# Performance work log

Hardware: AMD Instinct MI355X
Metric: run time of the kernel (lower is better)

## Reference

```python
import jax, jax.numpy as jnp
import numpy as np

N = 50000      # nodes
E = 800000     # edges (before self-loops)
IN = 64        # in_channels
H = 4          # heads
C = 32         # out_channels per head
HC = H * C     # 128
NEG_SLOPE = 0.2


def setup_inputs() -> dict:
    key = jax.random.key(0)
    ks = jax.random.split(key, 16)
    def p(k, shape):
        return (jax.random.normal(k, shape, jnp.float32) * 0.1)
    x = jax.random.normal(ks[0], (N, IN), jnp.float32)
    edge_index = jax.random.randint(ks[1], (2, E), 0, N, dtype=jnp.int32)
    return {
        "x": x,
        "Wl1": p(ks[2], (IN, HC)),  "bl1": p(ks[3], (HC,)),
        "Wr1": p(ks[4], (IN, HC)),  "br1": p(ks[5], (HC,)),
        "att1": p(ks[6], (H, C)),   "bias1": p(ks[7], (HC,)),
        "Wl2": p(ks[8], (HC, HC)),  "bl2": p(ks[9], (HC,)),
        "Wr2": p(ks[10], (HC, HC)), "br2": p(ks[11], (HC,)),
        "att2": p(ks[12], (H, C)),  "bias2": p(ks[13], (HC,)),
        "edge_index": edge_index,
    }


def gatv2_layer(x, src, dst, Wl, bl, Wr, br, att, bias):
    """GATv2Conv (concat=True, eval mode). src/dst include self-loops."""
    n = x.shape[0]
    h, c = att.shape
    xl = (x @ Wl + bl).reshape(n, h, c)   # source-side transform
    xr = (x @ Wr + br).reshape(n, h, c)   # target-side transform
    # per-edge GATv2 score: att . LeakyReLU(x_j + x_i)
    e = jax.nn.leaky_relu(xl[src] + xr[dst], NEG_SLOPE)   # [E', H, C]
    score = jnp.einsum('ehc,hc->eh', e, att)              # [E', H]
    # segment softmax over destination node
    m = jax.ops.segment_max(score, dst, num_segments=n)   # [N, H]
    ex = jnp.exp(score - m[dst])
    denom = jax.ops.segment_sum(ex, dst, num_segments=n)  # [N, H]
    alpha = ex / denom[dst]                               # [E', H]
    # weighted scatter-aggregate of source messages
    out = jax.ops.segment_sum(alpha[:, :, None] * xl[src], dst, num_segments=n)
    return out.reshape(n, h * c) + bias


def reference(x, Wl1, bl1, Wr1, br1, att1, bias1,
              Wl2, bl2, Wr2, br2, att2, bias2, edge_index):
    n = x.shape[0]
    loops = jnp.arange(n, dtype=edge_index.dtype)
    src = jnp.concatenate([edge_index[0], loops])  # PyG add_self_loops=True
    dst = jnp.concatenate([edge_index[1], loops])
    h = jax.nn.relu(gatv2_layer(x, src, dst, Wl1, bl1, Wr1, br1, att1, bias1))
    out = jax.nn.relu(gatv2_layer(h, src, dst, Wl2, bl2, Wr2, br2, att2, bias2))
    return out
```

## Files before the change

kernel.cpp:

```cpp
#include <hip/hip_runtime.h>

#define LEAKY 0.2f
#define NBSHIFT 8
#define TILE 4096

typedef __attribute__((ext_vector_type(8))) short  bfrag;
typedef __attribute__((ext_vector_type(4))) float  f32x4;

__device__ __forceinline__ unsigned bf16rne(float v) {
    unsigned u = __float_as_uint(v);
    return (u + 0x7FFF + ((u >> 16) & 1)) >> 16;
}
__device__ __forceinline__ float bf16tof(unsigned b) { return __uint_as_float(b << 16); }

#define DPPADD(p, ctrl)                                                       \
    p += __int_as_float(__builtin_amdgcn_mov_dpp(__float_as_int(p), ctrl,     \
                                                 0xF, 0xF, true))
__device__ __forceinline__ float rowsum8(float p) {
    DPPADD(p, 0xB1);
    DPPADD(p, 0x4E);
    DPPADD(p, 0x141);
    return p;
}


__global__ __launch_bounds__(256) void bucket_hist(const int* __restrict__ dst,
                                                   int* __restrict__ bcnt, int E, int nb) {
    __shared__ int h[256];
    h[threadIdx.x] = 0;
    __syncthreads();
    for (int e = blockIdx.x * 256 + threadIdx.x; e < E; e += gridDim.x * 256)
        atomicAdd(&h[dst[e] >> NBSHIFT], 1);
    __syncthreads();
    int v = h[threadIdx.x];
    if (threadIdx.x < nb && v) atomicAdd(&bcnt[threadIdx.x], v);
}

__global__ __launch_bounds__(256) void bucket_scan(const int* __restrict__ bcnt,
                                                   int* __restrict__ bbase,
                                                   int* __restrict__ gwoff,
                                                   int* __restrict__ rowptr,
                                                   int E, int nb, int n) {
    __shared__ int s[256];
    const int t = threadIdx.x;
    int v = (t < nb) ? bcnt[t] : 0;
    s[t] = v;
    __syncthreads();
    for (int off = 1; off < 256; off <<= 1) {
        int a = (t >= off) ? s[t - off] : 0;
        __syncthreads();
        s[t] += a;
        __syncthreads();
    }
    int excl = s[t] - v;
    if (t < nb) { bbase[t] = excl; gwoff[t] = excl; }
    if (t == 0) { bbase[nb] = E; rowptr[n] = E; }
}

__global__ __launch_bounds__(256) void multisplit(const int* __restrict__ src,
                                                  const int* __restrict__ dst,
                                                  int* __restrict__ gwoff,
                                                  int* __restrict__ pairs, int E, int nb) {
    __shared__ int hist[256], lofs[256], gb[256];
    __shared__ int st[TILE];
    const int t = threadIdx.x;
    const int tile0 = blockIdx.x * TILE;
    const int tend = min(tile0 + TILE, E);
    hist[t] = 0;
    __syncthreads();
    for (int e = tile0 + t; e < tend; e += 256)
        atomicAdd(&hist[dst[e] >> NBSHIFT], 1);
    __syncthreads();
    int v = hist[t];
    lofs[t] = v;
    __syncthreads();
    for (int off = 1; off < 256; off <<= 1) {
        int a = (t >= off) ? lofs[t - off] : 0;
        __syncthreads();
        lofs[t] += a;
        __syncthreads();
    }
    int excl = lofs[t] - v;
    __syncthreads();
    lofs[t] = excl;
    if (t < nb && v > 0) gb[t] = atomicAdd(&gwoff[t], v);
    hist[t] = 0;
    __syncthreads();
    for (int e = tile0 + t; e < tend; e += 256) {
        int d = dst[e];
        int b = d >> NBSHIFT;
        int r = atomicAdd(&hist[b], 1);
        st[lofs[b] + r] = (src[e] & 0xFFFF) | ((d & 255) << 16) | (b << 24);
    }
    __syncthreads();
    const int total = tend - tile0;
    for (int i = t; i < total; i += 256) {
        int p = st[i];
        int b = ((unsigned)p) >> 24;
        pairs[gb[b] + (i - lofs[b])] = p;
    }
}

__global__ __launch_bounds__(256) void bucket_sort(const int* __restrict__ pairs,
                                                   const int* __restrict__ bbase,
                                                   int* __restrict__ rowptr,
                                                   int* __restrict__ ssrc, int n) {
    __shared__ int hist[256], ofs[256];
    const int b = blockIdx.x, t = threadIdx.x;
    const int base = b << NBSHIFT;
    const int pbeg = bbase[b], pend = bbase[b + 1];
    hist[t] = 0;
    __syncthreads();
    for (int i = pbeg + t; i < pend; i += 256)
        atomicAdd(&hist[(pairs[i] >> 16) & 255], 1);
    __syncthreads();
    int v = hist[t];
    ofs[t] = v;
    __syncthreads();
    for (int off = 1; off < 256; off <<= 1) {
        int a = (t >= off) ? ofs[t - off] : 0;
        __syncthreads();
        ofs[t] += a;
        __syncthreads();
    }
    int excl = ofs[t] - v;
    __syncthreads();
    ofs[t] = excl;
    const int node = base + t;
    if (node < n) rowptr[node] = pbeg + excl;
    __syncthreads();
    for (int i = pbeg + t; i < pend; i += 256) {
        int p = pairs[i];
        int pos = atomicAdd(&ofs[(p >> 16) & 255], 1);
        ssrc[pbeg + pos] = p & 0xFFFF;
    }
}


__global__ void split_x(const float* __restrict__ x, ushort* __restrict__ xhi,
                        ushort* __restrict__ xlo, int total4) {
    int i = blockIdx.x * blockDim.x + threadIdx.x;
    if (i >= total4) return;
    float4 v = reinterpret_cast<const float4*>(x)[i];
    ushort4 h, l;
    float* vp = &v.x;
    ushort* hp = &h.x;
    ushort* lp = &l.x;
#pragma unroll
    for (int j = 0; j < 4; ++j) {
        unsigned hb = bf16rne(vp[j]);
        hp[j] = (ushort)hb;
        lp[j] = (ushort)bf16rne(vp[j] - bf16tof(hb));
    }
    reinterpret_cast<ushort4*>(xhi)[i] = h;
    reinterpret_cast<ushort4*>(xlo)[i] = l;
}


__global__ void pack_W(const float* __restrict__ Wl, const float* __restrict__ Wr,
                       ushort* __restrict__ Bhi, ushort* __restrict__ Blo, int K) {
    int tid = blockIdx.x * blockDim.x + threadIdx.x;
    if (tid >= K * 256) return;
    int k = tid >> 8;
    int c = tid & 255;
    float w = (c < 128) ? Wl[k * 128 + c] : Wr[k * 128 + (c - 128)];
    int s = k >> 5, kin = k & 31, kgrp = kin >> 3, j = kin & 7;
    int f = c >> 4, cin = c & 15;
    int lane = kgrp * 16 + cin;
    size_t pos = ((size_t)(s * 16 + f) * 64 + lane) * 8 + j;
    unsigned hb = bf16rne(w);
    Bhi[pos] = (ushort)hb;
    Blo[pos] = (ushort)bf16rne(w - bf16tof(hb));
}


template<int K>
__global__ __launch_bounds__(256) void gemm_mfma(
    const ushort* __restrict__ Ahi, const ushort* __restrict__ Alo,
    const ushort* __restrict__ Bhi, const ushort* __restrict__ Blo,
    const float* __restrict__ bl, const float* __restrict__ br,
    ushort* __restrict__ xlb, ushort* __restrict__ xrb, int n)
{
    __shared__ ushort BshH[2 * 8 * 64 * 8];
    __shared__ ushort BshL[2 * 8 * 64 * 8];
    const int t = threadIdx.x;
    const int w = t >> 6;
    const int lane = t & 63;
    const int half = blockIdx.y;
    const int r0 = blockIdx.x * 64 + w * 16;
    const int rl = lane & 15;
    const int kg = lane >> 4;
    int arow = r0 + rl; if (arow >= n) arow = 0;

    const float4* __restrict__ gH = reinterpret_cast<const float4*>(Bhi);
    const float4* __restrict__ gL = reinterpret_cast<const float4*>(Blo);
    float4* __restrict__ sH = reinterpret_cast<float4*>(BshH);
    float4* __restrict__ sL = reinterpret_cast<float4*>(BshL);

    f32x4 acc[8];
#pragma unroll
    for (int f = 0; f < 8; ++f) acc[f] = (f32x4){0.f, 0.f, 0.f, 0.f};

#pragma unroll
    for (int sg = 0; sg < K / 64; ++sg) {
        if (sg) __syncthreads();
#pragma unroll
        for (int i = t; i < 1024; i += 256) {
            int ss = i >> 9, fl = (i >> 6) & 7, ln = i & 63;
            int gidx = ((2 * sg + ss) * 16 + half * 8 + fl) * 64 + ln;
            sH[i] = gH[gidx];
            sL[i] = gL[gidx];
        }
        __syncthreads();

#pragma unroll
        for (int ss = 0; ss < 2; ++ss) {
            const int s = 2 * sg + ss;
            const size_t ao = (size_t)arow * K + s * 32 + kg * 8;
            bfrag ahi = *reinterpret_cast<const bfrag*>(&Ahi[ao]);
            bfrag alo = *reinterpret_cast<const bfrag*>(&Alo[ao]);
#pragma unroll
            for (int fl = 0; fl < 8; ++fl) {
                const int lofs = ((ss * 8 + fl) * 64 + lane) * 8;
                bfrag bhi = *reinterpret_cast<const bfrag*>(&BshH[lofs]);
                bfrag blo = *reinterpret_cast<const bfrag*>(&BshL[lofs]);
                acc[fl] = __builtin_amdgcn_mfma_f32_16x16x32_bf16(alo, bhi, acc[fl], 0, 0, 0);
                acc[fl] = __builtin_amdgcn_mfma_f32_16x16x32_bf16(ahi, blo, acc[fl], 0, 0, 0);
                acc[fl] = __builtin_amdgcn_mfma_f32_16x16x32_bf16(ahi, bhi, acc[fl], 0, 0, 0);
            }
        }
    }

    const int cin = lane & 15;
    const float* __restrict__ bias_ = half ? br : bl;
    ushort* __restrict__ outp = half ? xrb : xlb;
#pragma unroll
    for (int fl = 0; fl < 8; ++fl) {
        const int cc = fl * 16 + cin;
        const float bv = bias_[cc];
#pragma unroll
        for (int j = 0; j < 4; ++j) {
            const int rr = r0 + kg * 4 + j;
            if (rr < n)
                outp[(size_t)rr * 128 + cc] = (ushort)bf16rne(acc[fl][j] + bv);
        }
    }
}


template<int OUTMODE>
__global__ __launch_bounds__(256) void gat_agg(
    const ushort* __restrict__ xlb, const ushort* __restrict__ xrb,
    const float* __restrict__ att, const float* __restrict__ bias,
    const int* __restrict__ rowptr, const int* __restrict__ ssrc,
    float* __restrict__ out, ushort* __restrict__ ohi, ushort* __restrict__ olo,
    int n)
{
    const int node = blockIdx.x * 4 + (threadIdx.x >> 6);
    if (node >= n) return;
    const int lane = threadIdx.x & 63;
    const int m = lane & 31;
    const bool hiHalf = lane >= 32;

    const uint2* __restrict__ xlu = reinterpret_cast<const uint2*>(xlb);
    const float4 a4 = reinterpret_cast<const float4*>(att)[m];
    float4 xrv;
    {
        const uint2 u = reinterpret_cast<const uint2*>(xrb)[(size_t)node * 32 + m];
        xrv.x = __uint_as_float(u.x << 16);
        xrv.y = __uint_as_float(u.x & 0xFFFF0000u);
        xrv.z = __uint_as_float(u.y << 16);
        xrv.w = __uint_as_float(u.y & 0xFFFF0000u);
    }

    float den = 0.f;
    float4 acc = make_float4(0.f, 0.f, 0.f, 0.f);

#define GATHER(sA, sB) xlu[(size_t)(hiHalf ? (sB) : (sA)) * 32 + m]
#define PAIR(u, MSK)                                                  \
    {                                                                 \
        const float x0 = __uint_as_float((u).x << 16);                \
        const float x1 = __uint_as_float((u).x & 0xFFFF0000u);        \
        const float x2 = __uint_as_float((u).y << 16);                \
        const float x3 = __uint_as_float((u).y & 0xFFFF0000u);        \
        float e0 = x0 + xrv.x, e1 = x1 + xrv.y;                       \
        float e2 = x2 + xrv.z, e3 = x3 + xrv.w;                       \
        e0 = fmaxf(e0, LEAKY * e0);                                   \
        e1 = fmaxf(e1, LEAKY * e1);                                   \
        e2 = fmaxf(e2, LEAKY * e2);                                   \
        e3 = fmaxf(e3, LEAKY * e3);                                   \
        float p = e0 * a4.x + e1 * a4.y + e2 * a4.z + e3 * a4.w;      \
        p = rowsum8(p);                                               \
        float ex = __expf(p) MSK;                                     \
        den += ex;                                                    \
        acc.x += ex * x0; acc.y += ex * x1;                           \
        acc.z += ex * x2; acc.w += ex * x3;                           \
    }

    int i = rowptr[node];
    const int end = rowptr[node + 1];

    {
        const bool vB = i < end;
        const int sB = vB ? ssrc[i] : node;
        uint2 u = GATHER(node, sB);
        const float msk = (hiHalf && !vB) ? 0.f : 1.f;
        PAIR(u, * msk);
        if (vB) ++i;
    }

    for (; i + 8 <= end; i += 8) {
        int s0 = ssrc[i],     s1 = ssrc[i + 1], s2 = ssrc[i + 2], s3 = ssrc[i + 3];
        int s4 = ssrc[i + 4], s5 = ssrc[i + 5], s6 = ssrc[i + 6], s7 = ssrc[i + 7];
        uint2 u0 = GATHER(s0, s1);
        uint2 u1 = GATHER(s2, s3);
        uint2 u2 = GATHER(s4, s5);
        uint2 u3 = GATHER(s6, s7);
        PAIR(u0, );
        PAIR(u1, );
        PAIR(u2, );
        PAIR(u3, );
    }
    for (; i + 2 <= end; i += 2) {
        int s0 = ssrc[i], s1 = ssrc[i + 1];
        uint2 u = GATHER(s0, s1);
        PAIR(u, );
    }
    if (i < end) {
        int s0 = ssrc[i];
        uint2 u = GATHER(s0, s0);
        const float msk = hiHalf ? 0.f : 1.f;
        PAIR(u, * msk);
    }
#undef PAIR
#undef GATHER

    den   += __shfl_xor(den,   32);
    acc.x += __shfl_xor(acc.x, 32);
    acc.y += __shfl_xor(acc.y, 32);
    acc.z += __shfl_xor(acc.z, 32);
    acc.w += __shfl_xor(acc.w, 32);

    if (!hiHalf) {
        const float4 b4 = reinterpret_cast<const float4*>(bias)[m];
        const float r = 1.f / den;
        const float o0 = fmaxf(acc.x * r + b4.x, 0.f);
        const float o1 = fmaxf(acc.y * r + b4.y, 0.f);
        const float o2 = fmaxf(acc.z * r + b4.z, 0.f);
        const float o3 = fmaxf(acc.w * r + b4.w, 0.f);
        if (OUTMODE == 0) {
            reinterpret_cast<float4*>(out)[(size_t)node * 32 + m] =
                make_float4(o0, o1, o2, o3);
        } else {
            unsigned h0 = bf16rne(o0), h1 = bf16rne(o1);
            unsigned h2 = bf16rne(o2), h3 = bf16rne(o3);
            ushort4 hv = make_ushort4((ushort)h0, (ushort)h1, (ushort)h2, (ushort)h3);
            ushort4 lv = make_ushort4((ushort)bf16rne(o0 - bf16tof(h0)),
                                      (ushort)bf16rne(o1 - bf16tof(h1)),
                                      (ushort)bf16rne(o2 - bf16tof(h2)),
                                      (ushort)bf16rne(o3 - bf16tof(h3)));
            reinterpret_cast<ushort4*>(ohi)[(size_t)node * 32 + m] = hv;
            reinterpret_cast<ushort4*>(olo)[(size_t)node * 32 + m] = lv;
        }
    }
}


extern "C" void kernel_launch(void* const* d_in, const int* in_sizes, int n_in,
                              void* d_out, int out_size, void* d_ws, size_t ws_size,
                              hipStream_t stream)
{
    const float* x     = (const float*)d_in[0];
    const float* Wl1   = (const float*)d_in[1];
    const float* bl1   = (const float*)d_in[2];
    const float* Wr1   = (const float*)d_in[3];
    const float* br1   = (const float*)d_in[4];
    const float* att1  = (const float*)d_in[5];
    const float* bias1 = (const float*)d_in[6];
    const float* Wl2   = (const float*)d_in[7];
    const float* bl2   = (const float*)d_in[8];
    const float* Wr2   = (const float*)d_in[9];
    const float* br2   = (const float*)d_in[10];
    const float* att2  = (const float*)d_in[11];
    const float* bias2 = (const float*)d_in[12];
    const int*   eidx  = (const int*)d_in[13];

    const int n = in_sizes[0] / 64;
    const int E = in_sizes[13] / 2;
    const int* src = eidx;
    const int* dst = eidx + E;
    const int nb = (n + 255) >> 8;

    char* ws = (char*)d_ws;
    size_t off = 0;
    auto alloc = [&](size_t bytes) -> void* {
        void* p = ws + off;
        off = (off + bytes + 255) & ~(size_t)255;
        return p;
    };
    int* rowptr   = (int*)alloc((size_t)(n + 1) * 4);
    int* ssrc     = (int*)alloc((size_t)E * 4);
    int* bcnt     = (int*)alloc((size_t)nb * 4);
    int* bbase    = (int*)alloc((size_t)(nb + 1) * 4);
    int* gwoff    = (int*)alloc((size_t)nb * 4);
    ushort* B1hi  = (ushort*)alloc((size_t)64  * 256 * 2);
    ushort* B1lo  = (ushort*)alloc((size_t)64  * 256 * 2);
    ushort* B2hi  = (ushort*)alloc((size_t)128 * 256 * 2);
    ushort* B2lo  = (ushort*)alloc((size_t)128 * 256 * 2);
    ushort* xreg  = (ushort*)alloc((size_t)n * 128 * 2 * 2);
    ushort* xhi1  = xreg;
    ushort* xlo1  = xreg + (size_t)n * 64;
    ushort* hhi   = xreg;
    ushort* hlo   = xreg + (size_t)n * 128;
    ushort* xlb   = (ushort*)alloc((size_t)n * 128 * 2);
    ushort* xrb   = (ushort*)alloc((size_t)n * 128 * 2);
    int* pairs    = (int*)xlb;
    float* outp   = (float*)d_out;

    hipMemsetAsync(bcnt, 0, (size_t)nb * 4, stream);
    bucket_hist<<<128, 256, 0, stream>>>(dst, bcnt, E, nb);
    bucket_scan<<<1, 256, 0, stream>>>(bcnt, bbase, gwoff, rowptr, E, nb, n);
    multisplit<<<(E + TILE - 1) / TILE, 256, 0, stream>>>(src, dst, gwoff, pairs, E, nb);
    bucket_sort<<<nb, 256, 0, stream>>>(pairs, bbase, rowptr, ssrc, n);

    const int total4 = n * 64 / 4;
    split_x<<<(total4 + 255) / 256, 256, 0, stream>>>(x, xhi1, xlo1, total4);
    pack_W<<<(64  * 256 + 255) / 256, 256, 0, stream>>>(Wl1, Wr1, B1hi, B1lo, 64);
    pack_W<<<(128 * 256 + 255) / 256, 256, 0, stream>>>(Wl2, Wr2, B2hi, B2lo, 128);

    const dim3 ggrid((n + 63) / 64, 2);

    gemm_mfma<64><<<ggrid, 256, 0, stream>>>(xhi1, xlo1, B1hi, B1lo, bl1, br1,
                                             xlb, xrb, n);
    gat_agg<1><<<(n + 3) / 4, 256, 0, stream>>>(xlb, xrb, att1, bias1, rowptr, ssrc,
                                                nullptr, hhi, hlo, n);

    gemm_mfma<128><<<ggrid, 256, 0, stream>>>(hhi, hlo, B2hi, B2lo, bl2, br2,
                                              xlb, xrb, n);
    gat_agg<0><<<(n + 3) / 4, 256, 0, stream>>>(xlb, xrb, att2, bias2, rowptr, ssrc,
                                                outp, nullptr, nullptr, n);
}
```

Baseline: 193.0 us.

## Store layer-1 output as single bf16 and merge GEMM column halves per block

Layer-1 aggregation now writes the hidden activations as a single bf16 array instead of a hi/lo bf16 pair. The second GEMM therefore drops the A-low MFMA term, saving a third of its MFMAs and half of its A reads. The GEMM also covers both Wl and Wr column halves in one 512-thread block, so each A row is fetched once per block and the y-dimension of the grid goes away. The aggregation loop gains a 16-edge unrolled stage to put more gathers in flight, at the cost of lower precision in the layer-2 input.

```diff
diff --git a/kernel.cpp b/kernel.cpp
--- a/kernel.cpp
+++ b/kernel.cpp
@@ -174,20 +174,21 @@
 }
 
 
-template<int K>
-__global__ __launch_bounds__(256) void gemm_mfma(
+template<int K, bool SPLITA>
+__global__ __launch_bounds__(512) void gemm_mfma(
     const ushort* __restrict__ Ahi, const ushort* __restrict__ Alo,
     const ushort* __restrict__ Bhi, const ushort* __restrict__ Blo,
     const float* __restrict__ bl, const float* __restrict__ br,
     ushort* __restrict__ xlb, ushort* __restrict__ xrb, int n)
 {
-    __shared__ ushort BshH[2 * 8 * 64 * 8];
-    __shared__ ushort BshL[2 * 8 * 64 * 8];
+    __shared__ ushort BshH[2 * 16 * 64 * 8];
+    __shared__ ushort BshL[2 * 16 * 64 * 8];
     const int t = threadIdx.x;
     const int w = t >> 6;
     const int lane = t & 63;
-    const int half = blockIdx.y;
-    const int r0 = blockIdx.x * 64 + w * 16;
+    const int rfrag = w & 3;
+    const int chalf = w >> 2;
+    const int r0 = blockIdx.x * 64 + rfrag * 16;
     const int rl = lane & 15;
     const int kg = lane >> 4;
     int arow = r0 + rl; if (arow >= n) arow = 0;
@@ -205,9 +206,9 @@
     for (int sg = 0; sg < K / 64; ++sg) {
         if (sg) __syncthreads();
 #pragma unroll
-        for (int i = t; i < 1024; i += 256) {
-            int ss = i >> 9, fl = (i >> 6) & 7, ln = i & 63;
-            int gidx = ((2 * sg + ss) * 16 + half * 8 + fl) * 64 + ln;
+        for (int i = t; i < 2048; i += 512) {
+            int ss = i >> 10, fl = (i >> 6) & 15, ln = i & 63;
+            int gidx = ((2 * sg + ss) * 16 + fl) * 64 + ln;
             sH[i] = gH[gidx];
             sL[i] = gL[gidx];
         }
@@ -218,13 +219,15 @@
             const int s = 2 * sg + ss;
             const size_t ao = (size_t)arow * K + s * 32 + kg * 8;
             bfrag ahi = *reinterpret_cast<const bfrag*>(&Ahi[ao]);
-            bfrag alo = *reinterpret_cast<const bfrag*>(&Alo[ao]);
+            bfrag alo;
+            if (SPLITA) alo = *reinterpret_cast<const bfrag*>(&Alo[ao]);
 #pragma unroll
             for (int fl = 0; fl < 8; ++fl) {
-                const int lofs = ((ss * 8 + fl) * 64 + lane) * 8;
+                const int lofs = ((ss * 16 + chalf * 8 + fl) * 64 + lane) * 8;
                 bfrag bhi = *reinterpret_cast<const bfrag*>(&BshH[lofs]);
                 bfrag blo = *reinterpret_cast<const bfrag*>(&BshL[lofs]);
-                acc[fl] = __builtin_amdgcn_mfma_f32_16x16x32_bf16(alo, bhi, acc[fl], 0, 0, 0);
+                if (SPLITA)
+                    acc[fl] = __builtin_amdgcn_mfma_f32_16x16x32_bf16(alo, bhi, acc[fl], 0, 0, 0);
                 acc[fl] = __builtin_amdgcn_mfma_f32_16x16x32_bf16(ahi, blo, acc[fl], 0, 0, 0);
                 acc[fl] = __builtin_amdgcn_mfma_f32_16x16x32_bf16(ahi, bhi, acc[fl], 0, 0, 0);
             }
@@ -232,8 +235,8 @@
     }
 
     const int cin = lane & 15;
-    const float* __restrict__ bias_ = half ? br : bl;
-    ushort* __restrict__ outp = half ? xrb : xlb;
+    const float* __restrict__ bias_ = chalf ? br : bl;
+    ushort* __restrict__ outp = chalf ? xrb : xlb;
 #pragma unroll
     for (int fl = 0; fl < 8; ++fl) {
         const int cc = fl * 16 + cin;
@@ -253,8 +256,7 @@
     const ushort* __restrict__ xlb, const ushort* __restrict__ xrb,
     const float* __restrict__ att, const float* __restrict__ bias,
     const int* __restrict__ rowptr, const int* __restrict__ ssrc,
-    float* __restrict__ out, ushort* __restrict__ ohi, ushort* __restrict__ olo,
-    int n)
+    float* __restrict__ out, ushort* __restrict__ ob, int n)
 {
     const int node = blockIdx.x * 4 + (threadIdx.x >> 6);
     if (node >= n) return;
@@ -309,6 +311,22 @@
         if (vB) ++i;
     }
 
+    for (; i + 16 <= end; i += 16) {
+        int s0 = ssrc[i],      s1 = ssrc[i + 1],  s2 = ssrc[i + 2],  s3 = ssrc[i + 3];
+        int s4 = ssrc[i + 4],  s5 = ssrc[i + 5],  s6 = ssrc[i + 6],  s7 = ssrc[i + 7];
+        int s8 = ssrc[i + 8],  s9 = ssrc[i + 9],  sa = ssrc[i + 10], sb = ssrc[i + 11];
+        int sc = ssrc[i + 12], sd = ssrc[i + 13], se = ssrc[i + 14], sf = ssrc[i + 15];
+        uint2 u0 = GATHER(s0, s1);
+        uint2 u1 = GATHER(s2, s3);
+        uint2 u2 = GATHER(s4, s5);
+        uint2 u3 = GATHER(s6, s7);
+        uint2 u4 = GATHER(s8, s9);
+        uint2 u5 = GATHER(sa, sb);
+        uint2 u6 = GATHER(sc, sd);
+        uint2 u7 = GATHER(se, sf);
+        PAIR(u0, ); PAIR(u1, ); PAIR(u2, ); PAIR(u3, );
+        PAIR(u4, ); PAIR(u5, ); PAIR(u6, ); PAIR(u7, );
+    }
     for (; i + 8 <= end; i += 8) {
         int s0 = ssrc[i],     s1 = ssrc[i + 1], s2 = ssrc[i + 2], s3 = ssrc[i + 3];
         int s4 = ssrc[i + 4], s5 = ssrc[i + 5], s6 = ssrc[i + 6], s7 = ssrc[i + 7];
@@ -316,10 +334,7 @@
         uint2 u1 = GATHER(s2, s3);
         uint2 u2 = GATHER(s4, s5);
         uint2 u3 = GATHER(s6, s7);
-        PAIR(u0, );
-        PAIR(u1, );
-        PAIR(u2, );
-        PAIR(u3, );
+        PAIR(u0, ); PAIR(u1, ); PAIR(u2, ); PAIR(u3, );
     }
     for (; i + 2 <= end; i += 2) {
         int s0 = ssrc[i], s1 = ssrc[i + 1];
@@ -352,15 +367,9 @@
             reinterpret_cast<float4*>(out)[(size_t)node * 32 + m] =
                 make_float4(o0, o1, o2, o3);
         } else {
-            unsigned h0 = bf16rne(o0), h1 = bf16rne(o1);
-            unsigned h2 = bf16rne(o2), h3 = bf16rne(o3);
-            ushort4 hv = make_ushort4((ushort)h0, (ushort)h1, (ushort)h2, (ushort)h3);
-            ushort4 lv = make_ushort4((ushort)bf16rne(o0 - bf16tof(h0)),
-                                      (ushort)bf16rne(o1 - bf16tof(h1)),
-                                      (ushort)bf16rne(o2 - bf16tof(h2)),
-                                      (ushort)bf16rne(o3 - bf16tof(h3)));
-            reinterpret_cast<ushort4*>(ohi)[(size_t)node * 32 + m] = hv;
-            reinterpret_cast<ushort4*>(olo)[(size_t)node * 32 + m] = lv;
+            reinterpret_cast<ushort4*>(ob)[(size_t)node * 32 + m] =
+                make_ushort4((ushort)bf16rne(o0), (ushort)bf16rne(o1),
+                             (ushort)bf16rne(o2), (ushort)bf16rne(o3));
         }
     }
 }
@@ -407,11 +416,10 @@
     ushort* B1lo  = (ushort*)alloc((size_t)64  * 256 * 2);
     ushort* B2hi  = (ushort*)alloc((size_t)128 * 256 * 2);
     ushort* B2lo  = (ushort*)alloc((size_t)128 * 256 * 2);
-    ushort* xreg  = (ushort*)alloc((size_t)n * 128 * 2 * 2);
+    ushort* xreg  = (ushort*)alloc((size_t)n * 128 * 2);
     ushort* xhi1  = xreg;
     ushort* xlo1  = xreg + (size_t)n * 64;
-    ushort* hhi   = xreg;
-    ushort* hlo   = xreg + (size_t)n * 128;
+    ushort* hb    = xreg;
     ushort* xlb   = (ushort*)alloc((size_t)n * 128 * 2);
     ushort* xrb   = (ushort*)alloc((size_t)n * 128 * 2);
     int* pairs    = (int*)xlb;
@@ -428,15 +436,15 @@
     pack_W<<<(64  * 256 + 255) / 256, 256, 0, stream>>>(Wl1, Wr1, B1hi, B1lo, 64);
     pack_W<<<(128 * 256 + 255) / 256, 256, 0, stream>>>(Wl2, Wr2, B2hi, B2lo, 128);
 
-    const dim3 ggrid((n + 63) / 64, 2);
-
-    gemm_mfma<64><<<ggrid, 256, 0, stream>>>(xhi1, xlo1, B1hi, B1lo, bl1, br1,
-                                             xlb, xrb, n);
+    const int ggrid = (n + 63) / 64;
+
+    gemm_mfma<64, true><<<ggrid, 512, 0, stream>>>(xhi1, xlo1, B1hi, B1lo, bl1, br1,
+                                                   xlb, xrb, n);
     gat_agg<1><<<(n + 3) / 4, 256, 0, stream>>>(xlb, xrb, att1, bias1, rowptr, ssrc,
-                                                nullptr, hhi, hlo, n);
-
-    gemm_mfma<128><<<ggrid, 256, 0, stream>>>(hhi, hlo, B2hi, B2lo, bl2, br2,
-                                              xlb, xrb, n);
+                                                nullptr, hb, n);
+
+    gemm_mfma<128, false><<<ggrid, 512, 0, stream>>>(hb, hb, B2hi, B2lo, bl2, br2,
+                                                     xlb, xrb, n);
     gat_agg<0><<<(n + 3) / 4, 256, 0, stream>>>(xlb, xrb, att2, bias2, rowptr, ssrc,
-                                                outp, nullptr, nullptr, n);
-}
+                                                outp, nullptr, n);
+}
```

After: 214.5 us. 1.11x slower.
